# Kernel tuning notes

Measured on AMD Instinct MI355X. Metric: run time of the kernel, lower is better.

Reference implementation:

```python
import jax, jax.numpy as jnp
import numpy as np

INIT_STD = 0.02


def setup_inputs() -> dict:
    key = jax.random.key(0)
    kr, kq, kk, kv, ko = jax.random.split(key, 5)
    B, S, D = 4, 2048, 1024
    H, Dh = 16, 64
    residual = jax.random.normal(kr, (B, S, D), dtype=jnp.float32)
    W_Q = INIT_STD * jax.random.normal(kq, (H, Dh, D), dtype=jnp.float32)
    W_K = INIT_STD * jax.random.normal(kk, (H, Dh, D), dtype=jnp.float32)
    W_V = INIT_STD * jax.random.normal(kv, (H, Dh, D), dtype=jnp.float32)
    W_O = INIT_STD * jax.random.normal(ko, (H, Dh, D), dtype=jnp.float32)
    return {"residual": residual, "W_Q": W_Q, "W_K": W_K, "W_V": W_V, "W_O": W_O}


def reference(residual, W_Q, W_K, W_V, W_O):
    # residual: [b, s, m]; W_*: [h, d, m]
    d_head = W_Q.shape[1]
    seq_len = residual.shape[1]
    q = jnp.einsum('bsm,hdm->bshd', residual, W_Q)
    k = jnp.einsum('bsm,hdm->bshd', residual, W_K)
    v = jnp.einsum('bsm,hdm->bshd', residual, W_V)
    scores = jnp.einsum('bqhd,bkhd->bhqk', q, k) / jnp.sqrt(jnp.float32(d_head))
    causal = jnp.tril(jnp.ones((seq_len, seq_len), dtype=bool))
    scores = jnp.where(causal, scores, -jnp.inf)
    pattern = jax.nn.softmax(scores, axis=-1)  # [b, h, q, k]
    attn_out = jnp.einsum('bhqk,bkhd->bqhd', pattern, v)
    out = jnp.einsum('bqhd,hdm->bqm', attn_out, W_O)
    return out
```

## Files before the change

### kernel.cpp

```cpp
#include <hip/hip_runtime.h>
#include <stdint.h>

typedef unsigned short u16;
typedef __bf16 bf16x8 __attribute__((ext_vector_type(8)));
typedef float f32x4 __attribute__((ext_vector_type(4)));
typedef short s16x8 __attribute__((ext_vector_type(8)));
typedef short s16x4 __attribute__((ext_vector_type(4)));

__device__ __forceinline__ u16 f2bf(float f) {
  unsigned u = __float_as_uint(f);
  u += 0x7fff + ((u >> 16) & 1);
  return (u16)(u >> 16);
}

__device__ __forceinline__ void gld16(const void* g, void* l) {
  __builtin_amdgcn_global_load_lds((const __attribute__((address_space(1))) void*)g,
                                   (__attribute__((address_space(3))) void*)l, 16, 0, 0);
}

__global__ void cast_f32_bf16(const float* __restrict__ in, u16* __restrict__ out, int n) {
  int stride = gridDim.x * blockDim.x;
  for (int i = blockIdx.x * blockDim.x + threadIdx.x; i * 4 < n; i += stride) {
    f32x4 v = *(const f32x4*)(in + (size_t)i * 4);
    s16x4 o;
#pragma unroll
    for (int j = 0; j < 4; ++j) o[j] = (short)f2bf(v[j]);
    *(s16x4*)(out + (size_t)i * 4) = o;
  }
}

__global__ void transpose_cast(const float* __restrict__ in, u16* __restrict__ out, int R, int C) {
  int idx = blockIdx.x * 256 + threadIdx.x;
  if (idx < R * C) {
    int r = idx / C, c = idx - r * C;
    out[(size_t)c * R + r] = f2bf(in[idx]);
  }
}

template<int F32OUT>
__global__ __launch_bounds__(256, 3)
void gemm_bt(const u16* __restrict__ A, const u16* __restrict__ B,
             void* __restrict__ Cv, int M, int N, int K, int LDC) {
  __shared__ __align__(16) u16 As[128 * 64];
  __shared__ __align__(16) u16 Bs[128 * 64];
  const int tid = threadIdx.x;
  const int lane = tid & 63;
  const int wave = tid >> 6;
  const int wr = wave >> 1, wc = wave & 1;
  const int row0 = blockIdx.y * 128, col0 = blockIdx.x * 128;
  const u16* Ab = A + (size_t)row0 * K;
  const u16* Bb = B + (size_t)col0 * K;
  f32x4 acc[4][4] = {};
  for (int kt = 0; kt < K; kt += 64) {
#pragma unroll
    for (int i = 0; i < 4; ++i) {
      int c = i * 256 + tid;
      int o = c << 4;
      int row = o >> 7;
      int ol = o ^ ((row & 7) << 4);
      int colel = (ol & 127) >> 1;
      int ldsoff = (i * 256 + wave * 64) << 4;
      gld16(Ab + (size_t)row * K + kt + colel, (char*)As + ldsoff);
      gld16(Bb + (size_t)row * K + kt + colel, (char*)Bs + ldsoff);
    }
    __syncthreads();
#pragma unroll
    for (int ks = 0; ks < 2; ++ks) {
      const int kb = ks * 64 + ((lane >> 4) << 4);
      bf16x8 af[4], bfr[4];
#pragma unroll
      for (int m = 0; m < 4; ++m) {
        int r = wr * 64 + m * 16 + (lane & 15);
        int o = ((r << 7) + kb) ^ ((r & 7) << 4);
        af[m] = *(const bf16x8*)((const char*)As + o);
      }
#pragma unroll
      for (int n = 0; n < 4; ++n) {
        int r = wc * 64 + n * 16 + (lane & 15);
        int o = ((r << 7) + kb) ^ ((r & 7) << 4);
        bfr[n] = *(const bf16x8*)((const char*)Bs + o);
      }
#pragma unroll
      for (int m = 0; m < 4; ++m)
#pragma unroll
        for (int n = 0; n < 4; ++n)
          acc[m][n] = __builtin_amdgcn_mfma_f32_16x16x32_bf16(af[m], bfr[n], acc[m][n], 0, 0, 0);
    }
    __syncthreads();
  }
#pragma unroll
  for (int m = 0; m < 4; ++m) {
#pragma unroll
    for (int r = 0; r < 4; ++r) {
      int row = row0 + wr * 64 + m * 16 + ((lane >> 4) << 2) + r;
      int colb = col0 + wc * 64 + (lane & 15);
#pragma unroll
      for (int n = 0; n < 4; ++n) {
        float v = acc[m][n][r];
        if (F32OUT) ((float*)Cv)[(size_t)row * LDC + colb + n * 16] = v;
        else        ((u16*)Cv)[(size_t)row * LDC + colb + n * 16] = f2bf(v);
      }
    }
  }
}

__global__ __launch_bounds__(256, 2)
void attn_fwd(const u16* __restrict__ Qg, const u16* __restrict__ Kg,
              const u16* __restrict__ VTg, u16* __restrict__ Og,
              int S, int H, int LDV) {
  __shared__ __align__(16) u16 Kb[2][64 * 64];
  __shared__ __align__(16) u16 Vb[2][64 * 64];
  __shared__ __align__(16) u16 Ps[4][16 * 64];
  const int tid = threadIdx.x, lane = tid & 63, wave = tid >> 6;
  const int xcd = blockIdx.x & 7, t = blockIdx.x >> 3;
  const int pair = xcd * 8 + (t >> 3);
  const int j = t & 7;
  const int h = pair & 15, b = pair >> 4;
  const int D = H * 64;
  const int l15 = lane & 15, lg = lane >> 4;

  bf16x8 ones;
#pragma unroll
  for (int i = 0; i < 8; ++i) ones[i] = (__bf16)1.0f;

  for (int half = 0; half < 2; ++half) {
    const int qt = half ? j : (15 - j);
    const int q0 = qt * 128;
    const int wq0 = q0 + wave * 32;

    bf16x8 qf[2][2];
#pragma unroll
    for (int f = 0; f < 2; ++f) {
      const u16* qp = Qg + (size_t)(b * S + wq0 + f * 16 + l15) * D + h * 64 + (lg << 3);
      qf[f][0] = *(const bf16x8*)qp;
      qf[f][1] = *(const bf16x8*)(qp + 32);
    }

    f32x4 accO[2][4] = {};
    float mrow[2][4], lrow[2][4];
#pragma unroll
    for (int f = 0; f < 2; ++f)
#pragma unroll
      for (int r = 0; r < 4; ++r) { mrow[f][r] = -__builtin_inff(); lrow[f][r] = 0.f; }

    const int nkt = 2 * qt + 2;

    auto STAGE = [&](int kt, int bufi) {
      const int k0 = kt * 64;
#pragma unroll
      for (int i = 0; i < 2; ++i) {
        int c = i * 256 + tid;
        int o = c << 4;
        int row = o >> 7;
        int ol = o ^ ((row & 7) << 4);
        int colel = (ol & 127) >> 1;
        int ldsoff = i * 4096 + wave * 1024;
        gld16(Kg + (size_t)(b * S + k0 + row) * D + h * 64 + colel,
              (char*)&Kb[bufi][0] + ldsoff);
        gld16(VTg + (size_t)(h * 64 + row) * LDV + b * S + k0 + colel,
              (char*)&Vb[bufi][0] + ldsoff);
      }
    };

    STAGE(0, 0);
    __syncthreads();

    for (int kt = 0; kt < nkt; ++kt) {
      const int cur = kt & 1;
      if (kt + 1 < nkt) STAGE(kt + 1, cur ^ 1);

      const int k0 = kt * 64;
      if (k0 <= wq0 + 31) {
        f32x4 sf[2][4] = {};
        __builtin_amdgcn_s_setprio(1);
#pragma unroll
        for (int dstep = 0; dstep < 2; ++dstep) {
          const int kb = dstep * 64 + (lg << 4);
#pragma unroll
          for (int kf = 0; kf < 4; ++kf) {
            int r = kf * 16 + l15;
            int o = ((r << 7) + kb) ^ ((r & 7) << 4);
            bf16x8 k8 = *(const bf16x8*)((const char*)&Kb[cur][0] + o);
            sf[0][kf] = __builtin_amdgcn_mfma_f32_16x16x32_bf16(qf[0][dstep], k8, sf[0][kf], 0, 0, 0);
            sf[1][kf] = __builtin_amdgcn_mfma_f32_16x16x32_bf16(qf[1][dstep], k8, sf[1][kf], 0, 0, 0);
          }
        }
        __builtin_amdgcn_s_setprio(0);

        const bool needmask = (k0 + 63 > wq0);
#pragma unroll
        for (int f = 0; f < 2; ++f) {
          float rmax[4];
#pragma unroll
          for (int r = 0; r < 4; ++r) rmax[r] = -__builtin_inff();
          const int qbase = wq0 + f * 16 + (lg << 2);
#pragma unroll
          for (int kf = 0; kf < 4; ++kf) {
            int kcol = k0 + kf * 16 + l15;
#pragma unroll
            for (int r = 0; r < 4; ++r) {
              float s = sf[f][kf][r] * 0.125f;
              if (needmask && kcol > qbase + r) s = -__builtin_inff();
              sf[f][kf][r] = s;
              rmax[r] = fmaxf(rmax[r], s);
            }
          }
#pragma unroll
          for (int off = 1; off < 16; off <<= 1)
#pragma unroll
            for (int r = 0; r < 4; ++r)
              rmax[r] = fmaxf(rmax[r], __shfl_xor(rmax[r], off, 64));

          float need = -__builtin_inff();
#pragma unroll
          for (int r = 0; r < 4; ++r) need = fmaxf(need, rmax[r] - mrow[f][r]);
          float scl[4];
          if (__any(need > 8.f)) {
#pragma unroll
            for (int r = 0; r < 4; ++r) {
              float mnew = fmaxf(mrow[f][r], rmax[r]);
              scl[r] = __expf(mrow[f][r] - mnew);
              mrow[f][r] = mnew;
            }
#pragma unroll
            for (int df = 0; df < 4; ++df)
#pragma unroll
              for (int r = 0; r < 4; ++r) accO[f][df][r] *= scl[r];
          } else {
#pragma unroll
            for (int r = 0; r < 4; ++r) scl[r] = 1.f;
          }

#pragma unroll
          for (int kf = 0; kf < 4; ++kf) {
#pragma unroll
            for (int r = 0; r < 4; ++r) {
              float p = __expf(sf[f][kf][r] - mrow[f][r]);
              int prow = (lg << 2) + r;
              int pcol = kf * 16 + l15;
              int ob = ((prow << 7) + (pcol << 1)) ^ ((prow & 7) << 4);
              *(u16*)((char*)&Ps[wave][0] + ob) = f2bf(p);
            }
          }

          f32x4 ls = {};
          __builtin_amdgcn_s_setprio(1);
#pragma unroll
          for (int ks = 0; ks < 2; ++ks) {
            const int kb = ks * 64 + (lg << 4);
            int po = ((l15 << 7) + kb) ^ ((l15 & 7) << 4);
            bf16x8 pa = *(const bf16x8*)((const char*)&Ps[wave][0] + po);
            ls = __builtin_amdgcn_mfma_f32_16x16x32_bf16(pa, ones, ls, 0, 0, 0);
#pragma unroll
            for (int df = 0; df < 4; ++df) {
              int vr = df * 16 + l15;
              int vo = ((vr << 7) + kb) ^ ((vr & 7) << 4);
              bf16x8 v8 = *(const bf16x8*)((const char*)&Vb[cur][0] + vo);
              accO[f][df] = __builtin_amdgcn_mfma_f32_16x16x32_bf16(pa, v8, accO[f][df], 0, 0, 0);
            }
          }
          __builtin_amdgcn_s_setprio(0);
#pragma unroll
          for (int r = 0; r < 4; ++r) lrow[f][r] = lrow[f][r] * scl[r] + ls[r];
        }
      }
      __syncthreads();
    }

#pragma unroll
    for (int f = 0; f < 2; ++f) {
#pragma unroll
      for (int df = 0; df < 4; ++df) {
#pragma unroll
        for (int r = 0; r < 4; ++r) {
          int row = wq0 + f * 16 + (lg << 2) + r;
          int col = h * 64 + df * 16 + l15;
          Og[(size_t)(b * S + row) * D + col] = f2bf(accO[f][df][r] / lrow[f][r]);
        }
      }
    }
    __syncthreads();
  }
}

extern "C" void kernel_launch(void* const* d_in, const int* in_sizes, int n_in,
                              void* d_out, int out_size, void* d_ws, size_t ws_size,
                              hipStream_t stream) {
  const float* residual = (const float*)d_in[0];
  const float* W_Q = (const float*)d_in[1];
  const float* W_K = (const float*)d_in[2];
  const float* W_V = (const float*)d_in[3];
  const float* W_O = (const float*)d_in[4];
  float* out = (float*)d_out;
  const int B = 4, S = 2048, D = 1024, H = 16;
  const int M = B * S;
  const int LDV = M + 64;

  char* ws = (char*)d_ws;
  size_t off = 0;
  auto alloc = [&](size_t elems) {
    u16* p = (u16*)(ws + off);
    off += ((elems * 2 + 255) & ~(size_t)255);
    return p;
  };
  u16* resb = alloc((size_t)M * D);
  u16* Wqb  = alloc((size_t)D * D);
  u16* Wkb  = alloc((size_t)D * D);
  u16* Wvb  = alloc((size_t)D * D);
  u16* Wot  = alloc((size_t)D * D);
  u16* Qw   = alloc((size_t)M * D);
  u16* Kw   = alloc((size_t)M * D);
  u16* VT0  = alloc((size_t)D * LDV);
  u16* AOw  = resb;

  cast_f32_bf16<<<1024, 256, 0, stream>>>(residual, resb, M * D);
  cast_f32_bf16<<<256, 256, 0, stream>>>(W_Q, Wqb, D * D);
  cast_f32_bf16<<<256, 256, 0, stream>>>(W_K, Wkb, D * D);
  cast_f32_bf16<<<256, 256, 0, stream>>>(W_V, Wvb, D * D);
  transpose_cast<<<(D * D + 255) / 256, 256, 0, stream>>>(W_O, Wot, D, D);

  dim3 g(D / 128, M / 128);
  gemm_bt<0><<<g, 256, 0, stream>>>(resb, Wqb, Qw, M, D, D, D);
  gemm_bt<0><<<g, 256, 0, stream>>>(resb, Wkb, Kw, M, D, D, D);
  dim3 gv(M / 128, D / 128);
  gemm_bt<0><<<gv, 256, 0, stream>>>(Wvb, resb, VT0, D, M, D, LDV);

  attn_fwd<<<dim3(512), 256, 0, stream>>>(Qw, Kw, VT0, AOw, S, H, LDV);

  gemm_bt<1><<<g, 256, 0, stream>>>(AOw, Wot, out, M, D, D, D);
}
```

Baseline: 306.6 us.

## Use 8 waves of 16 query rows in attention; fold softmax scale into W_Q

The attention kernel now launches 512 threads per block, and each of the 8 waves owns 16 query rows instead of 32. Each thread issues one K/V load per stage instead of two. This lowers register pressure per wave, raises occupancy and splits causal work more finely across waves. The 1/sqrt(d) scale is folded into the W_Q bf16 cast, which removes a multiply per score but adds one extra bf16 rounding on Q. Each K tile is now shared by fewer query rows per wave, so fragment reuse drops.

```diff
diff --git a/kernel.cpp b/kernel.cpp
--- a/kernel.cpp
+++ b/kernel.cpp
@@ -25,6 +25,18 @@
     s16x4 o;
 #pragma unroll
     for (int j = 0; j < 4; ++j) o[j] = (short)f2bf(v[j]);
+    *(s16x4*)(out + (size_t)i * 4) = o;
+  }
+}
+
+__global__ void cast_f32_bf16_scale(const float* __restrict__ in, u16* __restrict__ out,
+                                    int n, float scale) {
+  int stride = gridDim.x * blockDim.x;
+  for (int i = blockIdx.x * blockDim.x + threadIdx.x; i * 4 < n; i += stride) {
+    f32x4 v = *(const f32x4*)(in + (size_t)i * 4);
+    s16x4 o;
+#pragma unroll
+    for (int j = 0; j < 4; ++j) o[j] = (short)f2bf(v[j] * scale);
     *(s16x4*)(out + (size_t)i * 4) = o;
   }
 }
@@ -104,13 +116,13 @@
   }
 }
 
-__global__ __launch_bounds__(256, 2)
+__global__ __launch_bounds__(512, 4)
 void attn_fwd(const u16* __restrict__ Qg, const u16* __restrict__ Kg,
               const u16* __restrict__ VTg, u16* __restrict__ Og,
               int S, int H, int LDV) {
   __shared__ __align__(16) u16 Kb[2][64 * 64];
   __shared__ __align__(16) u16 Vb[2][64 * 64];
-  __shared__ __align__(16) u16 Ps[4][16 * 64];
+  __shared__ __align__(16) u16 Ps[8][16 * 64];
   const int tid = threadIdx.x, lane = tid & 63, wave = tid >> 6;
   const int xcd = blockIdx.x & 7, t = blockIdx.x >> 3;
   const int pair = xcd * 8 + (t >> 3);
@@ -126,40 +138,30 @@
   for (int half = 0; half < 2; ++half) {
     const int qt = half ? j : (15 - j);
     const int q0 = qt * 128;
-    const int wq0 = q0 + wave * 32;
-
-    bf16x8 qf[2][2];
-#pragma unroll
-    for (int f = 0; f < 2; ++f) {
-      const u16* qp = Qg + (size_t)(b * S + wq0 + f * 16 + l15) * D + h * 64 + (lg << 3);
-      qf[f][0] = *(const bf16x8*)qp;
-      qf[f][1] = *(const bf16x8*)(qp + 32);
-    }
-
-    f32x4 accO[2][4] = {};
-    float mrow[2][4], lrow[2][4];
-#pragma unroll
-    for (int f = 0; f < 2; ++f)
-#pragma unroll
-      for (int r = 0; r < 4; ++r) { mrow[f][r] = -__builtin_inff(); lrow[f][r] = 0.f; }
+    const int wq0 = q0 + wave * 16;
+
+    const u16* qp = Qg + (size_t)(b * S + wq0 + l15) * D + h * 64 + (lg << 3);
+    bf16x8 qf0 = *(const bf16x8*)qp;
+    bf16x8 qf1 = *(const bf16x8*)(qp + 32);
+
+    f32x4 accO[4] = {};
+    float mrow[4], lrow[4];
+#pragma unroll
+    for (int r = 0; r < 4; ++r) { mrow[r] = -__builtin_inff(); lrow[r] = 0.f; }
 
     const int nkt = 2 * qt + 2;
 
     auto STAGE = [&](int kt, int bufi) {
       const int k0 = kt * 64;
-#pragma unroll
-      for (int i = 0; i < 2; ++i) {
-        int c = i * 256 + tid;
-        int o = c << 4;
-        int row = o >> 7;
-        int ol = o ^ ((row & 7) << 4);
-        int colel = (ol & 127) >> 1;
-        int ldsoff = i * 4096 + wave * 1024;
-        gld16(Kg + (size_t)(b * S + k0 + row) * D + h * 64 + colel,
-              (char*)&Kb[bufi][0] + ldsoff);
-        gld16(VTg + (size_t)(h * 64 + row) * LDV + b * S + k0 + colel,
-              (char*)&Vb[bufi][0] + ldsoff);
-      }
+      int o = tid << 4;
+      int row = o >> 7;
+      int ol = o ^ ((row & 7) << 4);
+      int colel = (ol & 127) >> 1;
+      int ldsoff = wave << 10;
+      gld16(Kg + (size_t)(b * S + k0 + row) * D + h * 64 + colel,
+            (char*)&Kb[bufi][0] + ldsoff);
+      gld16(VTg + (size_t)(h * 64 + row) * LDV + b * S + k0 + colel,
+            (char*)&Vb[bufi][0] + ldsoff);
     };
 
     STAGE(0, 0);
@@ -170,113 +172,113 @@
       if (kt + 1 < nkt) STAGE(kt + 1, cur ^ 1);
 
       const int k0 = kt * 64;
-      if (k0 <= wq0 + 31) {
-        f32x4 sf[2][4] = {};
+      if (k0 <= wq0 + 15) {
+        f32x4 sf[4] = {};
         __builtin_amdgcn_s_setprio(1);
 #pragma unroll
         for (int dstep = 0; dstep < 2; ++dstep) {
           const int kb = dstep * 64 + (lg << 4);
+          bf16x8 qa = dstep ? qf1 : qf0;
 #pragma unroll
           for (int kf = 0; kf < 4; ++kf) {
             int r = kf * 16 + l15;
             int o = ((r << 7) + kb) ^ ((r & 7) << 4);
             bf16x8 k8 = *(const bf16x8*)((const char*)&Kb[cur][0] + o);
-            sf[0][kf] = __builtin_amdgcn_mfma_f32_16x16x32_bf16(qf[0][dstep], k8, sf[0][kf], 0, 0, 0);
-            sf[1][kf] = __builtin_amdgcn_mfma_f32_16x16x32_bf16(qf[1][dstep], k8, sf[1][kf], 0, 0, 0);
+            sf[kf] = __builtin_amdgcn_mfma_f32_16x16x32_bf16(qa, k8, sf[kf], 0, 0, 0);
           }
         }
         __builtin_amdgcn_s_setprio(0);
 
-        const bool needmask = (k0 + 63 > wq0);
-#pragma unroll
-        for (int f = 0; f < 2; ++f) {
-          float rmax[4];
-#pragma unroll
-          for (int r = 0; r < 4; ++r) rmax[r] = -__builtin_inff();
-          const int qbase = wq0 + f * 16 + (lg << 2);
+        float rmax[4];
+#pragma unroll
+        for (int r = 0; r < 4; ++r) rmax[r] = -__builtin_inff();
+        const int qbase = wq0 + (lg << 2);
+        if (k0 + 63 > wq0) {
 #pragma unroll
           for (int kf = 0; kf < 4; ++kf) {
             int kcol = k0 + kf * 16 + l15;
 #pragma unroll
             for (int r = 0; r < 4; ++r) {
-              float s = sf[f][kf][r] * 0.125f;
-              if (needmask && kcol > qbase + r) s = -__builtin_inff();
-              sf[f][kf][r] = s;
+              float s = sf[kf][r];
+              if (kcol > qbase + r) s = -__builtin_inff();
+              sf[kf][r] = s;
               rmax[r] = fmaxf(rmax[r], s);
             }
           }
-#pragma unroll
-          for (int off = 1; off < 16; off <<= 1)
-#pragma unroll
-            for (int r = 0; r < 4; ++r)
-              rmax[r] = fmaxf(rmax[r], __shfl_xor(rmax[r], off, 64));
-
-          float need = -__builtin_inff();
-#pragma unroll
-          for (int r = 0; r < 4; ++r) need = fmaxf(need, rmax[r] - mrow[f][r]);
-          float scl[4];
-          if (__any(need > 8.f)) {
-#pragma unroll
-            for (int r = 0; r < 4; ++r) {
-              float mnew = fmaxf(mrow[f][r], rmax[r]);
-              scl[r] = __expf(mrow[f][r] - mnew);
-              mrow[f][r] = mnew;
-            }
-#pragma unroll
-            for (int df = 0; df < 4; ++df)
-#pragma unroll
-              for (int r = 0; r < 4; ++r) accO[f][df][r] *= scl[r];
-          } else {
-#pragma unroll
-            for (int r = 0; r < 4; ++r) scl[r] = 1.f;
-          }
-
-#pragma unroll
-          for (int kf = 0; kf < 4; ++kf) {
-#pragma unroll
-            for (int r = 0; r < 4; ++r) {
-              float p = __expf(sf[f][kf][r] - mrow[f][r]);
-              int prow = (lg << 2) + r;
-              int pcol = kf * 16 + l15;
-              int ob = ((prow << 7) + (pcol << 1)) ^ ((prow & 7) << 4);
-              *(u16*)((char*)&Ps[wave][0] + ob) = f2bf(p);
-            }
-          }
-
-          f32x4 ls = {};
-          __builtin_amdgcn_s_setprio(1);
-#pragma unroll
-          for (int ks = 0; ks < 2; ++ks) {
-            const int kb = ks * 64 + (lg << 4);
-            int po = ((l15 << 7) + kb) ^ ((l15 & 7) << 4);
-            bf16x8 pa = *(const bf16x8*)((const char*)&Ps[wave][0] + po);
-            ls = __builtin_amdgcn_mfma_f32_16x16x32_bf16(pa, ones, ls, 0, 0, 0);
-#pragma unroll
-            for (int df = 0; df < 4; ++df) {
-              int vr = df * 16 + l15;
-              int vo = ((vr << 7) + kb) ^ ((vr & 7) << 4);
-              bf16x8 v8 = *(const bf16x8*)((const char*)&Vb[cur][0] + vo);
-              accO[f][df] = __builtin_amdgcn_mfma_f32_16x16x32_bf16(pa, v8, accO[f][df], 0, 0, 0);
-            }
-          }
-          __builtin_amdgcn_s_setprio(0);
-#pragma unroll
-          for (int r = 0; r < 4; ++r) lrow[f][r] = lrow[f][r] * scl[r] + ls[r];
-        }
+        } else {
+#pragma unroll
+          for (int kf = 0; kf < 4; ++kf)
+#pragma unroll
+            for (int r = 0; r < 4; ++r) rmax[r] = fmaxf(rmax[r], sf[kf][r]);
+        }
+#pragma unroll
+        for (int off = 1; off < 16; off <<= 1)
+#pragma unroll
+          for (int r = 0; r < 4; ++r)
+            rmax[r] = fmaxf(rmax[r], __shfl_xor(rmax[r], off, 64));
+
+        float need = -__builtin_inff();
+#pragma unroll
+        for (int r = 0; r < 4; ++r) need = fmaxf(need, rmax[r] - mrow[r]);
+        float scl[4];
+        if (__any(need > 8.f)) {
+#pragma unroll
+          for (int r = 0; r < 4; ++r) {
+            float mnew = fmaxf(mrow[r], rmax[r]);
+            scl[r] = __expf(mrow[r] - mnew);
+            mrow[r] = mnew;
+          }
+#pragma unroll
+          for (int df = 0; df < 4; ++df)
+#pragma unroll
+            for (int r = 0; r < 4; ++r) accO[df][r] *= scl[r];
+        } else {
+#pragma unroll
+          for (int r = 0; r < 4; ++r) scl[r] = 1.f;
+        }
+
+#pragma unroll
+        for (int kf = 0; kf < 4; ++kf) {
+#pragma unroll
+          for (int r = 0; r < 4; ++r) {
+            float p = __expf(sf[kf][r] - mrow[r]);
+            int prow = (lg << 2) + r;
+            int pcol = kf * 16 + l15;
+            int ob = ((prow << 7) + (pcol << 1)) ^ ((prow & 7) << 4);
+            *(u16*)((char*)&Ps[wave][0] + ob) = f2bf(p);
+          }
+        }
+
+        f32x4 ls = {};
+        __builtin_amdgcn_s_setprio(1);
+#pragma unroll
+        for (int ks = 0; ks < 2; ++ks) {
+          const int kb = ks * 64 + (lg << 4);
+          int po = ((l15 << 7) + kb) ^ ((l15 & 7) << 4);
+          bf16x8 pa = *(const bf16x8*)((const char*)&Ps[wave][0] + po);
+          ls = __builtin_amdgcn_mfma_f32_16x16x32_bf16(pa, ones, ls, 0, 0, 0);
+#pragma unroll
+          for (int df = 0; df < 4; ++df) {
+            int vr = df * 16 + l15;
+            int vo = ((vr << 7) + kb) ^ ((vr & 7) << 4);
+            bf16x8 v8 = *(const bf16x8*)((const char*)&Vb[cur][0] + vo);
+            accO[df] = __builtin_amdgcn_mfma_f32_16x16x32_bf16(pa, v8, accO[df], 0, 0, 0);
+          }
+        }
+        __builtin_amdgcn_s_setprio(0);
+#pragma unroll
+        for (int r = 0; r < 4; ++r) lrow[r] = lrow[r] * scl[r] + ls[r];
       }
       __syncthreads();
     }
 
 #pragma unroll
-    for (int f = 0; f < 2; ++f) {
-#pragma unroll
-      for (int df = 0; df < 4; ++df) {
-#pragma unroll
-        for (int r = 0; r < 4; ++r) {
-          int row = wq0 + f * 16 + (lg << 2) + r;
-          int col = h * 64 + df * 16 + l15;
-          Og[(size_t)(b * S + row) * D + col] = f2bf(accO[f][df][r] / lrow[f][r]);
-        }
+    for (int df = 0; df < 4; ++df) {
+#pragma unroll
+      for (int r = 0; r < 4; ++r) {
+        int row = wq0 + (lg << 2) + r;
+        int col = h * 64 + df * 16 + l15;
+        Og[(size_t)(b * S + row) * D + col] = f2bf(accO[df][r] / lrow[r]);
       }
     }
     __syncthreads();
@@ -314,7 +316,7 @@
   u16* AOw  = resb;
 
   cast_f32_bf16<<<1024, 256, 0, stream>>>(residual, resb, M * D);
-  cast_f32_bf16<<<256, 256, 0, stream>>>(W_Q, Wqb, D * D);
+  cast_f32_bf16_scale<<<256, 256, 0, stream>>>(W_Q, Wqb, D * D, 0.125f);
   cast_f32_bf16<<<256, 256, 0, stream>>>(W_K, Wkb, D * D);
   cast_f32_bf16<<<256, 256, 0, stream>>>(W_V, Wvb, D * D);
   transpose_cast<<<(D * D + 255) / 256, 256, 0, stream>>>(W_O, Wot, D, D);
@@ -325,7 +327,7 @@
   dim3 gv(M / 128, D / 128);
   gemm_bt<0><<<gv, 256, 0, stream>>>(Wvb, resb, VT0, D, M, D, LDV);
 
-  attn_fwd<<<dim3(512), 256, 0, stream>>>(Qw, Kw, VT0, AOw, S, H, LDV);
+  attn_fwd<<<dim3(512), 512, 0, stream>>>(Qw, Kw, VT0, AOw, S, H, LDV);
 
   gemm_bt<1><<<g, 256, 0, stream>>>(AOw, Wot, out, M, D, D, D);
 }
```

Measured after the change: 291.4 us. 1.05x faster.
